# Performance work log

Hardware: AMD Instinct MI355X
Metric: run time of the kernel (lower is better)

The kernel has to match this reference:

```python
import jax, jax.numpy as jnp
import numpy as np

T, D = 256, 256
N, F, DM, H1, H2 = T + D, 2048, 512, 128, 64
E_HALF = T * D            # edges with src < dst (track -> detection)
LAM, SLACK = 5.0, -0.2    # hardcoded in original forward
SINK_ITERS = 8


def setup_inputs() -> dict:
    key = jax.random.key(0)
    ks = jax.random.split(key, 16)
    x = jax.random.normal(ks[0], (N, F), jnp.float32)
    coords = jax.random.normal(ks[1], (N, 4), jnp.float32)
    # boxes in xyxy with positive extent for IoU
    c = jax.random.uniform(ks[2], (N, 2), jnp.float32) * 0.8
    wh = jax.random.uniform(ks[3], (N, 2), jnp.float32) * 0.2 + 0.01
    coords_original = jnp.concatenate([c, c + wh], axis=1)
    ground_truth = (jax.random.uniform(ks[4], (E_HALF,)) < 0.1).astype(jnp.float32)
    # full bipartite directed edges: first half track->det (src<dst), second half reversed
    t = jnp.arange(T, dtype=jnp.int32)
    d = jnp.arange(D, dtype=jnp.int32) + T
    src_h = jnp.repeat(t, D)
    dst_h = jnp.tile(d, T)
    edge_index = jnp.stack([jnp.concatenate([src_h, dst_h]),
                            jnp.concatenate([dst_h, src_h])])

    def w(k, shape, fan_in):
        return jax.random.normal(k, shape, jnp.float32) / np.sqrt(fan_in).astype(np.float32)

    params = dict(
        W_enc=w(ks[5], (F, DM), F), b_enc=jnp.zeros((DM,), jnp.float32),
        app_W1=w(ks[6], (2 * DM, H1), 2 * DM), app_b1=jnp.zeros((H1,), jnp.float32),
        app_w2=w(ks[7], (H1,), H1), app_b2=jnp.zeros((), jnp.float32),
        geo_W1=w(ks[8], (8, H2), 8), geo_b1=jnp.zeros((H2,), jnp.float32),
        geo_w2=w(ks[9], (H2,), H2), geo_b2=jnp.zeros((), jnp.float32),
        aff_w=w(ks[10], (2,), 2), aff_b=jnp.zeros((), jnp.float32),
        W_self=w(ks[11], (DM, DM), DM), W_nbr=w(ks[12], (DM, DM), DM),
        b_mp=jnp.zeros((DM,), jnp.float32),
        fin_w=w(ks[13], (2,), 2), fin_b=jnp.zeros((), jnp.float32),
    )
    return dict(x=x, coords=coords, coords_original=coords_original,
                ground_truth=ground_truth, edge_index=edge_index, **params)


def _box_iou(a, b):
    # a, b: [E, 4] xyxy boxes
    lt = jnp.maximum(a[:, :2], b[:, :2])
    rb = jnp.minimum(a[:, 2:], b[:, 2:])
    wh = jnp.clip(rb - lt, 0.0)
    inter = wh[:, 0] * wh[:, 1]
    area_a = (a[:, 2] - a[:, 0]) * (a[:, 3] - a[:, 1])
    area_b = (b[:, 2] - b[:, 0]) * (b[:, 3] - b[:, 1])
    return inter / (area_a + area_b - inter + 1e-6)


def _forward(x, coords, coords_original, edge_index,
             W_enc, b_enc, app_W1, app_b1, app_w2, app_b2,
             geo_W1, geo_b1, geo_w2, geo_b2, aff_w, aff_b,
             W_self, W_nbr, b_mp, fin_w, fin_b):
    src, dst = edge_index[0], edge_index[1]
    # EncoderCNN -> node embeddings [N, DM]
    h = jax.nn.relu(x @ W_enc + b_enc)
    hs, hd = h[src], h[dst]                       # per-edge gathers [E, DM]
    # appearance affinity MLP on concat embeddings -> scalar per edge
    x1 = jax.nn.sigmoid(jax.nn.relu(jnp.concatenate([hs, hd], 1) @ app_W1 + app_b1) @ app_w2 + app_b2)
    # geometric affinity MLP on concat coords -> scalar per edge
    geo = jnp.concatenate([coords[src], coords[dst]], 1)   # [E, 8]
    x2 = jax.nn.sigmoid(jax.nn.relu(geo @ geo_W1 + geo_b1) @ geo_w2 + geo_b2)
    iou = _box_iou(coords_original[src], coords_original[dst])   # [E]
    # combine -> edge weight (affinityNet)
    ew = jax.nn.sigmoid(jnp.stack([x1, x2], axis=-1) @ aff_w + aff_b)  # [E]
    # optimNet: weighted message passing -> updated node embeddings
    agg = jax.ops.segment_sum(ew[:, None] * (hs @ W_nbr), dst, num_segments=N)
    out = jax.nn.relu(h @ W_self + agg + b_mp)    # [N, DM]
    # edges with src < dst are exactly the first E_HALF by construction
    a, b = out[src[:E_HALF]], out[dst[:E_HALF]]
    na = jnp.clip(jnp.linalg.norm(a, axis=1), 1e-6)
    nb = jnp.clip(jnp.linalg.norm(b, axis=1), 1e-6)
    cos = jnp.sum(a * b, axis=1) / (na * nb)
    fin = jax.nn.sigmoid(jnp.stack([cos, iou[:E_HALF]], axis=-1) @ fin_w + fin_b)  # [E_HALF]
    # scatter-built cost matrix with slack row/column, Sinkhorn normalization
    sv = jnp.exp(jnp.float32(SLACK * LAM))
    M = jnp.zeros((T + 1, D + 1), jnp.float32)
    M = M.at[src[:E_HALF], dst[:E_HALF] - T].set(jnp.exp(fin * LAM))
    M = M.at[:, D].set(sv)
    M = M.at[T, :].set(sv)
    for _ in range(SINK_ITERS):
        M = M / jnp.sum(M, axis=1, keepdims=True)
        M = M / jnp.sum(M, axis=0, keepdims=True)
    return M[:T, :D].reshape(-1)   # [T*D]


def reference(x, coords, coords_original, ground_truth, edge_index,
              W_enc, b_enc, app_W1, app_b1, app_w2, app_b2,
              geo_W1, geo_b1, geo_w2, geo_b2, aff_w, aff_b,
              W_self, W_nbr, b_mp, fin_w, fin_b):
    normalized = _forward(x, coords, coords_original, edge_index,
                          W_enc, b_enc, app_W1, app_b1, app_w2, app_b2,
                          geo_W1, geo_b1, geo_w2, geo_b2, aff_w, aff_b,
                          W_self, W_nbr, b_mp, fin_w, fin_b)
    # post-Sinkhorn entries are strictly positive, so the !=0 filter is identity
    det_num = jnp.full((1,), D, jnp.int32)
    tracklet_num = jnp.full((1,), T, jnp.int32)
    return normalized, ground_truth, det_num, tracklet_num
```

## Files before the change

kernel.cpp:

```cpp
#include <hip/hip_runtime.h>
#include <hip/hip_fp16.h>
#include <math.h>

#define EH   65536
#define LAMF 5.0f
#define SVF  0.36787944117144233f

typedef __bf16 bf16x8 __attribute__((ext_vector_type(8)));
typedef float  f32x4  __attribute__((ext_vector_type(4)));
typedef _Float16 f16x2 __attribute__((ext_vector_type(2)));

__device__ __forceinline__ float sigmoidf_(float x) { return 1.0f / (1.0f + expf(-x)); }

__device__ __forceinline__ void cvt1(float v, ushort& h, ushort& l) {
    __bf16 bh = (__bf16)v;
    h = __builtin_bit_cast(ushort, bh);
    __bf16 bl = (__bf16)(v - (float)bh);
    l = __builtin_bit_cast(ushort, bl);
}

__device__ __forceinline__ f16x2 u2h(uint u) { return __builtin_bit_cast(f16x2, u); }
__device__ __forceinline__ float2 h2f2u(uint u) {
    __half2 h = __builtin_bit_cast(__half2, u);
    return __half22float2(h);
}

#define LSTR 40
template<int MODE>
__global__ __launch_bounds__(256) void gemm64(
    const float* __restrict__ Aa, const float* __restrict__ Ab,
    const float* __restrict__ B0, const float* __restrict__ B1,
    const float* __restrict__ B2,
    const float* __restrict__ HsC45, const float* __restrict__ bmp,
    float* __restrict__ C0, float* __restrict__ C1)
{
    __shared__ ushort As_hi[64*LSTR], As_lo[64*LSTR], Bs_hi[64*LSTR], Bs_lo[64*LSTR];
    const int tid = threadIdx.x;
    const int row0 = blockIdx.y * 64;

    const float* Ap = Aa; int lda, arow0 = row0, ak = 0;
    const float* Bp; int ldb, kb = 0, bcol0;
    float* Cp; int ldc, ccol0;
    int KS;

    if (MODE == 0) {
        KS = 256; lda = 2048; ak = blockIdx.z * 256;
        Bp = B0; ldb = 512; kb = blockIdx.z * 256; bcol0 = blockIdx.x * 64;
        Cp = C0 + blockIdx.z * 262144; ldc = 512; ccol0 = bcol0;
    } else if (MODE == 1) {
        KS = 512; lda = 512;
        int cb = blockIdx.x;
        if (cb < 8)       { Bp=B0; ldb=512; kb=0;   bcol0=cb*64;        Cp=C0; ldc=1024; ccol0=cb*64; }
        else if (cb < 16) { Bp=B1; ldb=512; kb=0;   bcol0=(cb-8)*64;    Cp=C0; ldc=1024; ccol0=512+(cb-8)*64; }
        else if (cb < 18) { Bp=B2; ldb=128; kb=0;   bcol0=(cb-16)*64;   Cp=C1; ldc=256;  ccol0=(cb-16)*64; }
        else              { Bp=B2; ldb=128; kb=512; bcol0=(cb-18)*64;   Cp=C1; ldc=256;  ccol0=128+(cb-18)*64; }
    } else {
        KS = 256; lda = 256;
        if (row0 < 256) { Ap = Aa; arow0 = row0;       kb = 256; }
        else            { Ap = Ab; arow0 = row0 - 256; kb = 0; }
        Bp = B0; ldb = 1024; bcol0 = blockIdx.x * 64;
        Cp = C0; ldc = 512; ccol0 = bcol0;
    }

    const int arow = tid >> 2, kq = (tid & 3) * 8;
    const int kr = (tid & 15) * 2, nc0 = (tid >> 4) * 4;
    const float* aptr = Ap + (size_t)(arow0 + arow) * lda + ak + kq;
    const float* bptr = Bp + (size_t)(kb + kr) * ldb + bcol0 + nc0;

    f32x4 acc[2][2] = {};
    const int lane = tid & 63, w = tid >> 6;
    const int qr = (w >> 1) * 32, qc = (w & 1) * 32;
    const int fr = lane & 15, kg = (lane >> 4) * 8;

    float4 pa0, pa1, pb0, pb1;
    pa0 = *(const float4*)aptr; pa1 = *(const float4*)(aptr + 4);
    pb0 = *(const float4*)bptr; pb1 = *(const float4*)(bptr + ldb);

    for (int k0 = 0; k0 < KS; k0 += 32) {
        {
            ushort4 h0, l0, h1, l1;
            cvt1(pa0.x,h0.x,l0.x); cvt1(pa0.y,h0.y,l0.y); cvt1(pa0.z,h0.z,l0.z); cvt1(pa0.w,h0.w,l0.w);
            cvt1(pa1.x,h1.x,l1.x); cvt1(pa1.y,h1.y,l1.y); cvt1(pa1.z,h1.z,l1.z); cvt1(pa1.w,h1.w,l1.w);
            *(ushort4*)&As_hi[arow*LSTR + kq]     = h0;
            *(ushort4*)&As_hi[arow*LSTR + kq + 4] = h1;
            *(ushort4*)&As_lo[arow*LSTR + kq]     = l0;
            *(ushort4*)&As_lo[arow*LSTR + kq + 4] = l1;
            float b0a[4] = {pb0.x, pb0.y, pb0.z, pb0.w};
            float b1a[4] = {pb1.x, pb1.y, pb1.z, pb1.w};
            #pragma unroll
            for (int j = 0; j < 4; ++j) {
                ushort ha, la, hb, lb;
                cvt1(b0a[j], ha, la); cvt1(b1a[j], hb, lb);
                *(uint*)&Bs_hi[(nc0+j)*LSTR + kr] = (uint)ha | ((uint)hb << 16);
                *(uint*)&Bs_lo[(nc0+j)*LSTR + kr] = (uint)la | ((uint)lb << 16);
            }
        }
        __syncthreads();
        if (k0 + 32 < KS) {
            pa0 = *(const float4*)(aptr + k0 + 32);
            pa1 = *(const float4*)(aptr + k0 + 36);
            const float* bp2 = bptr + (size_t)(k0 + 32) * ldb;
            pb0 = *(const float4*)bp2; pb1 = *(const float4*)(bp2 + ldb);
        }
        bf16x8 ah[2], al[2], bh[2], bl[2];
        #pragma unroll
        for (int m = 0; m < 2; ++m) {
            int r = (qr + m*16 + fr) * LSTR + kg;
            ah[m] = *(const bf16x8*)&As_hi[r];
            al[m] = *(const bf16x8*)&As_lo[r];
        }
        #pragma unroll
        for (int n = 0; n < 2; ++n) {
            int r = (qc + n*16 + fr) * LSTR + kg;
            bh[n] = *(const bf16x8*)&Bs_hi[r];
            bl[n] = *(const bf16x8*)&Bs_lo[r];
        }
        #pragma unroll
        for (int m = 0; m < 2; ++m)
            #pragma unroll
            for (int n = 0; n < 2; ++n) {
                acc[m][n] = __builtin_amdgcn_mfma_f32_16x16x32_bf16(ah[m], bh[n], acc[m][n], 0, 0, 0);
                acc[m][n] = __builtin_amdgcn_mfma_f32_16x16x32_bf16(ah[m], bl[n], acc[m][n], 0, 0, 0);
                acc[m][n] = __builtin_amdgcn_mfma_f32_16x16x32_bf16(al[m], bh[n], acc[m][n], 0, 0, 0);
            }
        __syncthreads();
    }

    const int rbase = (lane >> 4) * 4;
    #pragma unroll
    for (int m = 0; m < 2; ++m)
        #pragma unroll
        for (int n = 0; n < 2; ++n)
            #pragma unroll
            for (int r = 0; r < 4; ++r) {
                int gr = row0 + qr + m*16 + rbase + r;
                int gc = ccol0 + qc + n*16 + (lane & 15);
                float v = acc[m][n][r];
                if (MODE == 2) {
                    v += HsC45[(size_t)gr * 1024 + 512 + gc] + bmp[gc];
                    v = fmaxf(v, 0.f);
                }
                Cp[(size_t)gr * ldc + gc] = v;
            }
}

__global__ __launch_bounds__(256) void enc_reduce(const float* __restrict__ P,
    const float* __restrict__ bias, float* __restrict__ h)
{
    int e = (blockIdx.x * 256 + threadIdx.x) * 4;
    int col = e & 511;
    float4 s = *(const float4*)&P[e];
    #pragma unroll
    for (int z = 1; z < 8; ++z) {
        float4 v = *(const float4*)&P[e + z * 262144];
        s.x += v.x; s.y += v.y; s.z += v.z; s.w += v.w;
    }
    float4 b = *(const float4*)&bias[col];
    float4 o;
    o.x = fmaxf(s.x + b.x, 0.f);
    o.y = fmaxf(s.y + b.y, 0.f);
    o.z = fmaxf(s.z + b.z, 0.f);
    o.w = fmaxf(s.w + b.w, 0.f);
    *(float4*)&h[e] = o;
}

__global__ __launch_bounds__(256) void edge_geo_kernel(
    const float* __restrict__ C23, const float* __restrict__ coords,
    const float* __restrict__ geo_W1, const float* __restrict__ geo_b1,
    const float* __restrict__ app_b1, const float* __restrict__ app_w2,
    const float* __restrict__ app_b2, const float* __restrict__ geo_w2,
    const float* __restrict__ geo_b2, const float* __restrict__ aff_w,
    const float* __restrict__ aff_b, const float* __restrict__ co,
    const float* __restrict__ gt, float* __restrict__ outp,
    float* __restrict__ ewT0, float* __restrict__ ew2, float* __restrict__ iou1)
{
    __shared__ __align__(16) float sA[16][132], sB[16][132];
    __shared__ __align__(16) float sGA[16][68], sGB[16][68];
    __shared__ __align__(16) float sw2[128], sgw2[64];
    __shared__ float sgw[8][64], sgb[64], scs[16][4], scd[16][4];
    const int tid = threadIdx.x;
    const int half = blockIdx.z;
    const int t0 = blockIdx.y * 16, d0 = blockIdx.x * 16;
    const int sbase = half ? (256 + d0) : t0;
    const int dbase = half ? t0 : (256 + d0);

    if (half == 1) {
        int bid = blockIdx.y * 16 + blockIdx.x;
        if (tid < 64) {
            int o = bid * 256 + tid * 4;
            *(float4*)&outp[EH + o] = *(const float4*)&gt[o];
        }
        if (bid == 0 && tid == 64) {
            outp[2 * EH]     = 256.0f;
            outp[2 * EH + 1] = 256.0f;
        }
    }

    for (int i = tid; i < 16 * 32; i += 256) {
        int rr = i >> 5, c4 = (i & 31) << 2;
        float4 va = *(const float4*)&C23[(sbase + rr) * 256 + c4];
        sA[rr][c4] = va.x; sA[rr][c4+1] = va.y; sA[rr][c4+2] = va.z; sA[rr][c4+3] = va.w;
        float4 vb = *(const float4*)&C23[(dbase + rr) * 256 + 128 + c4];
        float4 b1 = *(const float4*)&app_b1[c4];
        sB[rr][c4] = vb.x + b1.x; sB[rr][c4+1] = vb.y + b1.y;
        sB[rr][c4+2] = vb.z + b1.z; sB[rr][c4+3] = vb.w + b1.w;
    }
    for (int i = tid; i < 512; i += 256) sgw[i >> 6][i & 63] = geo_W1[i];
    if (tid < 64) sgb[tid] = geo_b1[tid];
    else if (tid < 192) sw2[tid - 64] = app_w2[tid - 64];
    else sgw2[tid - 192] = geo_w2[tid - 192];
    if (tid < 64) scs[tid >> 2][tid & 3] = coords[(sbase + (tid >> 2)) * 4 + (tid & 3)];
    else if (tid < 128) { int i = tid - 64; scd[i >> 2][i & 3] = coords[(dbase + (i >> 2)) * 4 + (i & 3)]; }
    __syncthreads();
    for (int v = tid; v < 2048; v += 256) {
        int hh = v >> 10, rr = (v >> 6) & 15, j = v & 63;
        if (hh == 0) {
            sGA[rr][j] = scs[rr][0]*sgw[0][j] + scs[rr][1]*sgw[1][j]
                       + scs[rr][2]*sgw[2][j] + scs[rr][3]*sgw[3][j] + sgb[j];
        } else {
            sGB[rr][j] = scd[rr][0]*sgw[4][j] + scd[rr][1]*sgw[5][j]
                       + scd[rr][2]*sgw[6][j] + scd[rr][3]*sgw[7][j];
        }
    }
    __syncthreads();
    const int tx = tid & 15, ty = tid >> 4;
    const int si = half ? tx : ty;
    const int di = half ? ty : tx;
    float acc1 = 0.f;
    #pragma unroll
    for (int j4 = 0; j4 < 128; j4 += 4) {
        float4 a = *(const float4*)&sA[si][j4];
        float4 b = *(const float4*)&sB[di][j4];
        float4 wv = *(const float4*)&sw2[j4];
        acc1 += fmaxf(a.x + b.x, 0.f) * wv.x + fmaxf(a.y + b.y, 0.f) * wv.y
              + fmaxf(a.z + b.z, 0.f) * wv.z + fmaxf(a.w + b.w, 0.f) * wv.w;
    }
    float x1 = sigmoidf_(acc1 + app_b2[0]);
    float acc2 = 0.f;
    #pragma unroll
    for (int j4 = 0; j4 < 64; j4 += 4) {
        float4 a = *(const float4*)&sGA[si][j4];
        float4 b = *(const float4*)&sGB[di][j4];
        float4 wv = *(const float4*)&sgw2[j4];
        acc2 += fmaxf(a.x + b.x, 0.f) * wv.x + fmaxf(a.y + b.y, 0.f) * wv.y
              + fmaxf(a.z + b.z, 0.f) * wv.z + fmaxf(a.w + b.w, 0.f) * wv.w;
    }
    float x2 = sigmoidf_(acc2 + geo_b2[0]);
    float e = sigmoidf_(x1 * aff_w[0] + x2 * aff_w[1] + aff_b[0]);
    const int t = t0 + ty, d = d0 + tx;
    if (half) ew2[t * 256 + d] = e;
    else      ewT0[d * 256 + t] = e;
    if (half == 0) {
        float4 a = *(const float4*)&co[t * 4];
        float4 b = *(const float4*)&co[(256 + d) * 4];
        float ltx = fmaxf(a.x, b.x), lty = fmaxf(a.y, b.y);
        float rbx = fminf(a.z, b.z), rby = fminf(a.w, b.w);
        float w  = fmaxf(rbx - ltx, 0.f), hh = fmaxf(rby - lty, 0.f);
        float inter = w * hh;
        float areaA = (a.z - a.x) * (a.w - a.y);
        float areaB = (b.z - b.x) * (b.w - b.y);
        iou1[t * 256 + d] = inter / (areaA + areaB - inter + 1e-6f);
    }
}

__global__ __launch_bounds__(256) void gram32(const float* __restrict__ outm,
    const float* __restrict__ iou, const float* __restrict__ finw,
    const float* __restrict__ finb, __half* __restrict__ Mh)
{
    __shared__ ushort As_hi[32*LSTR], As_lo[32*LSTR], Bs_hi[32*LSTR], Bs_lo[32*LSTR];
    __shared__ float snA[32], snB[32];
    const int tid = threadIdx.x;
    const int t0 = blockIdx.y * 32, d0 = blockIdx.x * 32;
    const float* Asrc = outm;
    const float* Bsrc = outm + (size_t)256 * 512;

    const int arow = tid >> 3, kq = (tid & 7) * 4;
    const float* aptr = Asrc + (size_t)(t0 + arow) * 512 + kq;
    const float* bptr = Bsrc + (size_t)(d0 + arow) * 512 + kq;

    f32x4 acc = {};
    float ssA = 0.f, ssB = 0.f;
    const int lane = tid & 63, w = tid >> 6;
    const int qr = (w >> 1) * 16, qc = (w & 1) * 16;
    const int fr = lane & 15, kg = (lane >> 4) * 8;

    float4 pa = *(const float4*)aptr;
    float4 pb = *(const float4*)bptr;

    for (int k0 = 0; k0 < 512; k0 += 32) {
        ssA += pa.x*pa.x + pa.y*pa.y + pa.z*pa.z + pa.w*pa.w;
        ssB += pb.x*pb.x + pb.y*pb.y + pb.z*pb.z + pb.w*pb.w;
        {
            ushort4 h4, l4;
            cvt1(pa.x,h4.x,l4.x); cvt1(pa.y,h4.y,l4.y); cvt1(pa.z,h4.z,l4.z); cvt1(pa.w,h4.w,l4.w);
            *(ushort4*)&As_hi[arow*LSTR + kq] = h4;
            *(ushort4*)&As_lo[arow*LSTR + kq] = l4;
            cvt1(pb.x,h4.x,l4.x); cvt1(pb.y,h4.y,l4.y); cvt1(pb.z,h4.z,l4.z); cvt1(pb.w,h4.w,l4.w);
            *(ushort4*)&Bs_hi[arow*LSTR + kq] = h4;
            *(ushort4*)&Bs_lo[arow*LSTR + kq] = l4;
        }
        __syncthreads();
        if (k0 + 32 < 512) {
            pa = *(const float4*)(aptr + k0 + 32);
            pb = *(const float4*)(bptr + k0 + 32);
        }
        bf16x8 ah, al, bh, bl;
        {
            int r = (qr + fr) * LSTR + kg;
            ah = *(const bf16x8*)&As_hi[r]; al = *(const bf16x8*)&As_lo[r];
        }
        {
            int r = (qc + fr) * LSTR + kg;
            bh = *(const bf16x8*)&Bs_hi[r]; bl = *(const bf16x8*)&Bs_lo[r];
        }
        acc = __builtin_amdgcn_mfma_f32_16x16x32_bf16(ah, bh, acc, 0, 0, 0);
        acc = __builtin_amdgcn_mfma_f32_16x16x32_bf16(ah, bl, acc, 0, 0, 0);
        acc = __builtin_amdgcn_mfma_f32_16x16x32_bf16(al, bh, acc, 0, 0, 0);
        __syncthreads();
    }
    ssA += __shfl_xor(ssA, 1); ssA += __shfl_xor(ssA, 2); ssA += __shfl_xor(ssA, 4);
    ssB += __shfl_xor(ssB, 1); ssB += __shfl_xor(ssB, 2); ssB += __shfl_xor(ssB, 4);
    if ((tid & 7) == 0) { snA[arow] = ssA; snB[arow] = ssB; }
    __syncthreads();
    const float fw0 = finw[0], fw1 = finw[1], fb = finb[0];
    const int rbase = (lane >> 4) * 4, lc = qc + (lane & 15);
    #pragma unroll
    for (int r = 0; r < 4; ++r) {
        int lr = qr + rbase + r;
        float na = fmaxf(sqrtf(snA[lr]), 1e-6f);
        float nb = fmaxf(sqrtf(snB[lc]), 1e-6f);
        int t = t0 + lr, d = d0 + lc;
        float cosv = acc[r] / (na * nb);
        float fin = sigmoidf_(cosv * fw0 + iou[t * 256 + d] * fw1 + fb);
        Mh[t * 256 + d] = __float2half(expf(fin * LAMF));
    }
}

__global__ __launch_bounds__(1024, 4) void sinkhorn4f(const __half* __restrict__ Mh,
    float* __restrict__ out)
{
    __shared__ __align__(16) float r_f[256], c_f[256];
    __shared__ float red[16];
    __shared__ __half r_h[256], c_h[256];
    const int tid = threadIdx.x;
    const int row = tid >> 2, sub4 = tid & 3;
    const int cg = tid >> 5, sub32 = tid & 31;

    const uint4* gm = (const uint4*)Mh;
    uint4 mr[8];
    #pragma unroll
    for (int j = 0; j < 8; ++j) mr[j] = gm[row * 32 + sub4 * 8 + j];
    uint4 mca[4], mcb[4];
    #pragma unroll
    for (int p = 0; p < 4; ++p) {
        int rp = 2 * sub32 + 64 * p;
        mca[p] = gm[rp * 32 + cg];
        mcb[p] = gm[(rp + 1) * 32 + cg];
    }
    if (tid < 256) { c_f[tid] = 1.0f; c_h[tid] = __float2half(1.0f); }
    if (tid == 0) red[1] = 1.0f / SVF;
    __syncthreads();

    const int b4 = (sub32 >> 4) & 1, b3 = (sub32 >> 3) & 1, b2 = (sub32 >> 2) & 1;

    for (int it = 0; it < 8; ++it) {
        float c256 = 1.0f / (SVF * red[1]);
        float a0 = 0.f, a1 = 0.f, a2 = 0.f, a3 = 0.f;
        {
            uint4 cu[4];
            #pragma unroll
            for (int j = 0; j < 4; ++j) cu[j] = *(const uint4*)&c_h[sub4 * 64 + j * 8];
            #pragma unroll
// ... 18 lines not shown
        if (tid < 64) {
            float s = c_f[tid] + c_f[tid + 64] + c_f[tid + 128] + c_f[tid + 192];
            #pragma unroll
            for (int o = 32; o; o >>= 1) s += __shfl_down(s, o);
            if (tid == 0) red[0] = s + c256;
        }
        if (sub4 == 0) {
            float v = 1.0f / (acc + SVF * c256);
            r_f[row] = v; r_h[row] = __float2half(v);
        }
        __syncthreads();

        float r256 = 1.0f / (SVF * red[0]);
        float b[8] = {0.f,0.f,0.f,0.f,0.f,0.f,0.f,0.f};
        #pragma unroll
        for (int p = 0; p < 4; ++p) {
            f16x2 rp = u2h(*(const uint*)&r_h[2 * sub32 + 64 * p]);
            uint lo, hi;
            lo = __builtin_amdgcn_perm(mcb[p].x, mca[p].x, 0x05040100);
            hi = __builtin_amdgcn_perm(mcb[p].x, mca[p].x, 0x07060302);
            b[0] = __builtin_amdgcn_fdot2(u2h(lo), rp, b[0], false);
            b[1] = __builtin_amdgcn_fdot2(u2h(hi), rp, b[1], false);
            lo = __builtin_amdgcn_perm(mcb[p].y, mca[p].y, 0x05040100);
            hi = __builtin_amdgcn_perm(mcb[p].y, mca[p].y, 0x07060302);
            b[2] = __builtin_amdgcn_fdot2(u2h(lo), rp, b[2], false);
            b[3] = __builtin_amdgcn_fdot2(u2h(hi), rp, b[3], false);
            lo = __builtin_amdgcn_perm(mcb[p].z, mca[p].z, 0x05040100);
            hi = __builtin_amdgcn_perm(mcb[p].z, mca[p].z, 0x07060302);
            b[4] = __builtin_amdgcn_fdot2(u2h(lo), rp, b[4], false);
            b[5] = __builtin_amdgcn_fdot2(u2h(hi), rp, b[5], false);
            lo = __builtin_amdgcn_perm(mcb[p].w, mca[p].w, 0x05040100);
            hi = __builtin_amdgcn_perm(mcb[p].w, mca[p].w, 0x07060302);
            b[6] = __builtin_amdgcn_fdot2(u2h(lo), rp, b[6], false);
            b[7] = __builtin_amdgcn_fdot2(u2h(hi), rp, b[7], false);
        }
        float t0v, t1v, t2v, t3v;
        t0v = b4 ? b[0] : b[4]; t1v = b4 ? b[1] : b[5];
        t2v = b4 ? b[2] : b[6]; t3v = b4 ? b[3] : b[7];
        t0v = __shfl_xor(t0v, 16); t1v = __shfl_xor(t1v, 16);
        t2v = __shfl_xor(t2v, 16); t3v = __shfl_xor(t3v, 16);
        float k0 = (b4 ? b[4] : b[0]) + t0v;
        float k1 = (b4 ? b[5] : b[1]) + t1v;
        float k2 = (b4 ? b[6] : b[2]) + t2v;
        float k3 = (b4 ? b[7] : b[3]) + t3v;
        float u0 = b3 ? k0 : k2, u1 = b3 ? k1 : k3;
        u0 = __shfl_xor(u0, 8); u1 = __shfl_xor(u1, 8);
        float m0 = (b3 ? k2 : k0) + u0;
        float m1 = (b3 ? k3 : k1) + u1;
        float w0 = b2 ? m0 : m1;
        w0 = __shfl_xor(w0, 4);
        float s = (b2 ? m1 : m0) + w0;
        s += __shfl_xor(s, 1); s += __shfl_xor(s, 2);
        if (tid < 64) {
            float s2 = r_f[tid] + r_f[tid + 64] + r_f[tid + 128] + r_f[tid + 192];
            #pragma unroll
            for (int o = 32; o; o >>= 1) s2 += __shfl_down(s2, o);
            if (tid == 0) red[1] = s2 + r256;
        }
        if ((sub32 & 3) == 0) {
            int col = cg * 8 + b4 * 4 + b3 * 2 + b2;
            float v = 1.0f / (s + SVF * r256);
            c_f[col] = v; c_h[col] = __float2half(v);
        }
        __syncthreads();
    }

    float rv = r_f[row];
    #pragma unroll
    for (int j = 0; j < 8; ++j) {
        int cb = sub4 * 64 + j * 8;
        float4 ca  = *(const float4*)&c_f[cb];
        float4 cb4 = *(const float4*)&c_f[cb + 4];
        float2 f0 = h2f2u(mr[j].x), f1 = h2f2u(mr[j].y);
        float2 f2 = h2f2u(mr[j].z), f3 = h2f2u(mr[j].w);
        float4 o0, o1;
        o0.x = f0.x * rv * ca.x;  o0.y = f0.y * rv * ca.y;
        o0.z = f1.x * rv * ca.z;  o0.w = f1.y * rv * ca.w;
        o1.x = f2.x * rv * cb4.x; o1.y = f2.y * rv * cb4.y;
        o1.z = f3.x * rv * cb4.z; o1.w = f3.y * rv * cb4.w;
        *(float4*)&out[row * 256 + cb]     = o0;
        *(float4*)&out[row * 256 + cb + 4] = o1;
    }
}

extern "C" void kernel_launch(void* const* d_in, const int* in_sizes, int n_in,
                              void* d_out, int out_size, void* d_ws, size_t ws_size,
                              hipStream_t stream)
{
    const float* x       = (const float*)d_in[0];
    const float* coords  = (const float*)d_in[1];
    const float* co      = (const float*)d_in[2];
    const float* gt      = (const float*)d_in[3];
    const float* W_enc   = (const float*)d_in[5];
    const float* b_enc   = (const float*)d_in[6];
    const float* app_W1  = (const float*)d_in[7];
    const float* app_b1  = (const float*)d_in[8];
    const float* app_w2  = (const float*)d_in[9];
    const float* app_b2  = (const float*)d_in[10];
    const float* geo_W1  = (const float*)d_in[11];
    const float* geo_b1  = (const float*)d_in[12];
    const float* geo_w2  = (const float*)d_in[13];
    const float* geo_b2  = (const float*)d_in[14];
    const float* aff_w   = (const float*)d_in[15];
    const float* aff_b   = (const float*)d_in[16];
    const float* W_self  = (const float*)d_in[17];
    const float* W_nbr   = (const float*)d_in[18];
    const float* b_mp    = (const float*)d_in[19];
    const float* fin_w   = (const float*)d_in[20];
    const float* fin_b   = (const float*)d_in[21];
    float* out = (float*)d_out;

    char* W = (char*)d_ws;
    float*  P     = (float*)(W + 0);
    float*  h     = (float*)(W + 8388608);
    float*  C45   = (float*)(W + 0);
    float*  C23   = (float*)(W + 2097152);
    float*  ewT0  = (float*)(W + 2621440);
    float*  ew2   = (float*)(W + 2883584);
    float*  iou1  = (float*)(W + 3145728);
    __half* Mh    = (__half*)(W + 3407872);
    float*  outm  = (float*)(W + 3670016);

    gemm64<0><<<dim3(8, 8, 8), 256, 0, stream>>>(x, nullptr, W_enc, nullptr, nullptr,
        nullptr, nullptr, P, nullptr);
    enc_reduce<<<256, 256, 0, stream>>>(P, b_enc, h);
    gemm64<1><<<dim3(20, 8), 256, 0, stream>>>(h, nullptr, W_nbr, W_self, app_W1,
        nullptr, nullptr, C45, C23);
    edge_geo_kernel<<<dim3(16, 16, 2), 256, 0, stream>>>(C23, coords, geo_W1, geo_b1,
        app_b1, app_w2, app_b2, geo_w2, geo_b2, aff_w, aff_b, co, gt, out,
        ewT0, ew2, iou1);
    gemm64<2><<<dim3(8, 8), 256, 0, stream>>>(ew2, ewT0, C45, nullptr, nullptr,
        C45, b_mp, outm, nullptr);
    gram32<<<dim3(8, 8), 256, 0, stream>>>(outm, iou1, fin_w, fin_b, Mh);
    sinkhorn4f<<<1, 1024, 0, stream>>>(Mh, out);
}
```

Before: 90.96 us.

## Fuse pipeline stages into one cooperative persistent kernel with grid syncs

```diff
diff --git a/kernel.cpp b/kernel.cpp
--- a/kernel.cpp
+++ b/kernel.cpp
@@ -1,6 +1,9 @@
 #include <hip/hip_runtime.h>
+#include <hip/hip_cooperative_groups.h>
 #include <hip/hip_fp16.h>
 #include <math.h>
+
+namespace cg = cooperative_groups;
 
 #define EH   65536
 #define LAMF 5.0f
@@ -26,46 +29,62 @@
 }
 
 #define LSTR 40
+
+struct GemmS {
+    ushort As_hi[64*LSTR], As_lo[64*LSTR], Bs_hi[64*LSTR], Bs_lo[64*LSTR];
+};
+struct EdgeS {
+    float sA[16][132], sB[16][132];
+    float sGA[16][68], sGB[16][68];
+    float sw2[128], sgw2[64];
+    float sgw[8][64], sgb[64];
+    float scs[16][4], scd[16][4];
+};
+struct GramS {
+    ushort As_hi[32*LSTR], As_lo[32*LSTR], Bs_hi[32*LSTR], Bs_lo[32*LSTR];
+    float snA[32], snB[32];
+};
+#define SMEM_BYTES 29184
+
 template<int MODE>
-__global__ __launch_bounds__(256) void gemm64(
+__device__ void gemm_phase(char* smem_, int bid,
     const float* __restrict__ Aa, const float* __restrict__ Ab,
     const float* __restrict__ B0, const float* __restrict__ B1,
-    const float* __restrict__ B2,
+    const float* __restrict__ B2, const float* __restrict__ bias,
     const float* __restrict__ HsC45, const float* __restrict__ bmp,
     float* __restrict__ C0, float* __restrict__ C1)
 {
-    __shared__ ushort As_hi[64*LSTR], As_lo[64*LSTR], Bs_hi[64*LSTR], Bs_lo[64*LSTR];
+    GemmS* S = (GemmS*)smem_;
     const int tid = threadIdx.x;
-    const int row0 = blockIdx.y * 64;
-
-    const float* Ap = Aa; int lda, arow0 = row0, ak = 0;
-    const float* Bp; int ldb, kb = 0, bcol0;
-    float* Cp; int ldc, ccol0;
-    int KS;
+
+    int row0, arow0, ak = 0, kb = 0, bcol0, ldb, ldc, ccol0, KS, lda;
+    const float* Ap = Aa; const float* Bp; float* Cp;
 
     if (MODE == 0) {
-        KS = 256; lda = 2048; ak = blockIdx.z * 256;
-        Bp = B0; ldb = 512; kb = blockIdx.z * 256; bcol0 = blockIdx.x * 64;
-        Cp = C0 + blockIdx.z * 262144; ldc = 512; ccol0 = bcol0;
+        int z = bid >> 6, by = (bid >> 3) & 7, bx = bid & 7;
+        row0 = by * 64; arow0 = row0; KS = 512; lda = 2048; ak = z * 512;
+        Bp = B0; ldb = 512; kb = z * 512; bcol0 = bx * 64;
+        Cp = C0 + z * 262144; ldc = 512; ccol0 = bcol0;
     } else if (MODE == 1) {
-        KS = 512; lda = 512;
-        int cb = blockIdx.x;
-        if (cb < 8)       { Bp=B0; ldb=512; kb=0;   bcol0=cb*64;        Cp=C0; ldc=1024; ccol0=cb*64; }
-        else if (cb < 16) { Bp=B1; ldb=512; kb=0;   bcol0=(cb-8)*64;    Cp=C0; ldc=1024; ccol0=512+(cb-8)*64; }
-        else if (cb < 18) { Bp=B2; ldb=128; kb=0;   bcol0=(cb-16)*64;   Cp=C1; ldc=256;  ccol0=(cb-16)*64; }
-        else              { Bp=B2; ldb=128; kb=512; bcol0=(cb-18)*64;   Cp=C1; ldc=256;  ccol0=128+(cb-18)*64; }
+        int by = bid / 20, cb = bid % 20;
+        row0 = by * 64; arow0 = row0; KS = 512; lda = 512;
+        if (cb < 8)       { Bp=B0; ldb=512; kb=0;   bcol0=cb*64;      Cp=C0; ldc=1024; ccol0=cb*64; }
+        else if (cb < 16) { Bp=B1; ldb=512; kb=0;   bcol0=(cb-8)*64;  Cp=C0; ldc=1024; ccol0=512+(cb-8)*64; }
+        else if (cb < 18) { Bp=B2; ldb=128; kb=0;   bcol0=(cb-16)*64; Cp=C1; ldc=256;  ccol0=(cb-16)*64; }
+        else              { Bp=B2; ldb=128; kb=512; bcol0=(cb-18)*64; Cp=C1; ldc=256;  ccol0=128+(cb-18)*64; }
     } else {
-        KS = 256; lda = 256;
+        int by = bid >> 3, bx = bid & 7;
+        row0 = by * 64; KS = 256; lda = 256;
         if (row0 < 256) { Ap = Aa; arow0 = row0;       kb = 256; }
         else            { Ap = Ab; arow0 = row0 - 256; kb = 0; }
-        Bp = B0; ldb = 1024; bcol0 = blockIdx.x * 64;
-        Cp = C0; ldc = 512; ccol0 = bcol0;
+        Bp = B0; ldb = 1024; bcol0 = bx * 64; Cp = C0; ldc = 512; ccol0 = bcol0;
     }
 
     const int arow = tid >> 2, kq = (tid & 3) * 8;
     const int kr = (tid & 15) * 2, nc0 = (tid >> 4) * 4;
-    const float* aptr = Ap + (size_t)(arow0 + arow) * lda + ak + kq;
-    const float* bptr = Bp + (size_t)(kb + kr) * ldb + bcol0 + nc0;
+    const float* aptr  = Ap + (size_t)(arow0 + arow) * lda + ak + kq;
+    const float* aptrP = Aa + (size_t)(arow0 + arow) * 512 + kq;
+    const float* bptr  = Bp + (size_t)(kb + kr) * ldb + bcol0 + nc0;
 
     f32x4 acc[2][2] = {};
     const int lane = tid & 63, w = tid >> 6;
@@ -73,32 +92,62 @@
     const int fr = lane & 15, kg = (lane >> 4) * 8;
 
     float4 pa0, pa1, pb0, pb1;
-    pa0 = *(const float4*)aptr; pa1 = *(const float4*)(aptr + 4);
+    float4 pz0[4], pz1[4];
+    if constexpr (MODE == 1) {
+        #pragma unroll
+        for (int z = 0; z < 4; ++z) {
+            pz0[z] = *(const float4*)(aptrP + z * 262144);
+            pz1[z] = *(const float4*)(aptrP + z * 262144 + 4);
+        }
+    } else {
+        pa0 = *(const float4*)aptr; pa1 = *(const float4*)(aptr + 4);
+    }
     pb0 = *(const float4*)bptr; pb1 = *(const float4*)(bptr + ldb);
 
     for (int k0 = 0; k0 < KS; k0 += 32) {
+        float4 sa0, sa1;
+        if constexpr (MODE == 1) {
+            float4 b0v = *(const float4*)&bias[k0 + kq];
+            float4 b1v = *(const float4*)&bias[k0 + kq + 4];
+            sa0.x = fmaxf(pz0[0].x + pz0[1].x + pz0[2].x + pz0[3].x + b0v.x, 0.f);
+            sa0.y = fmaxf(pz0[0].y + pz0[1].y + pz0[2].y + pz0[3].y + b0v.y, 0.f);
+            sa0.z = fmaxf(pz0[0].z + pz0[1].z + pz0[2].z + pz0[3].z + b0v.z, 0.f);
+            sa0.w = fmaxf(pz0[0].w + pz0[1].w + pz0[2].w + pz0[3].w + b0v.w, 0.f);
+            sa1.x = fmaxf(pz1[0].x + pz1[1].x + pz1[2].x + pz1[3].x + b1v.x, 0.f);
+            sa1.y = fmaxf(pz1[0].y + pz1[1].y + pz1[2].y + pz1[3].y + b1v.y, 0.f);
+            sa1.z = fmaxf(pz1[0].z + pz1[1].z + pz1[2].z + pz1[3].z + b1v.z, 0.f);
+            sa1.w = fmaxf(pz1[0].w + pz1[1].w + pz1[2].w + pz1[3].w + b1v.w, 0.f);
+        } else { sa0 = pa0; sa1 = pa1; }
         {
             ushort4 h0, l0, h1, l1;
-            cvt1(pa0.x,h0.x,l0.x); cvt1(pa0.y,h0.y,l0.y); cvt1(pa0.z,h0.z,l0.z); cvt1(pa0.w,h0.w,l0.w);
-            cvt1(pa1.x,h1.x,l1.x); cvt1(pa1.y,h1.y,l1.y); cvt1(pa1.z,h1.z,l1.z); cvt1(pa1.w,h1.w,l1.w);
-            *(ushort4*)&As_hi[arow*LSTR + kq]     = h0;
-            *(ushort4*)&As_hi[arow*LSTR + kq + 4] = h1;
-            *(ushort4*)&As_lo[arow*LSTR + kq]     = l0;
-            *(ushort4*)&As_lo[arow*LSTR + kq + 4] = l1;
+            cvt1(sa0.x,h0.x,l0.x); cvt1(sa0.y,h0.y,l0.y); cvt1(sa0.z,h0.z,l0.z); cvt1(sa0.w,h0.w,l0.w);
+            cvt1(sa1.x,h1.x,l1.x); cvt1(sa1.y,h1.y,l1.y); cvt1(sa1.z,h1.z,l1.z); cvt1(sa1.w,h1.w,l1.w);
+            *(ushort4*)&S->As_hi[arow*LSTR + kq]     = h0;
+            *(ushort4*)&S->As_hi[arow*LSTR + kq + 4] = h1;
+            *(ushort4*)&S->As_lo[arow*LSTR + kq]     = l0;
+            *(ushort4*)&S->As_lo[arow*LSTR + kq + 4] = l1;
             float b0a[4] = {pb0.x, pb0.y, pb0.z, pb0.w};
             float b1a[4] = {pb1.x, pb1.y, pb1.z, pb1.w};
             #pragma unroll
             for (int j = 0; j < 4; ++j) {
                 ushort ha, la, hb, lb;
                 cvt1(b0a[j], ha, la); cvt1(b1a[j], hb, lb);
-                *(uint*)&Bs_hi[(nc0+j)*LSTR + kr] = (uint)ha | ((uint)hb << 16);
-                *(uint*)&Bs_lo[(nc0+j)*LSTR + kr] = (uint)la | ((uint)lb << 16);
+                *(uint*)&S->Bs_hi[(nc0+j)*LSTR + kr] = (uint)ha | ((uint)hb << 16);
+                *(uint*)&S->Bs_lo[(nc0+j)*LSTR + kr] = (uint)la | ((uint)lb << 16);
             }
         }
         __syncthreads();
         if (k0 + 32 < KS) {
-            pa0 = *(const float4*)(aptr + k0 + 32);
-            pa1 = *(const float4*)(aptr + k0 + 36);
+            if constexpr (MODE == 1) {
+                #pragma unroll
+                for (int z = 0; z < 4; ++z) {
+                    pz0[z] = *(const float4*)(aptrP + z * 262144 + k0 + 32);
+                    pz1[z] = *(const float4*)(aptrP + z * 262144 + k0 + 36);
+                }
+            } else {
+                pa0 = *(const float4*)(aptr + k0 + 32);
+                pa1 = *(const float4*)(aptr + k0 + 36);
+            }
             const float* bp2 = bptr + (size_t)(k0 + 32) * ldb;
             pb0 = *(const float4*)bp2; pb1 = *(const float4*)(bp2 + ldb);
         }
@@ -106,14 +155,14 @@
         #pragma unroll
         for (int m = 0; m < 2; ++m) {
             int r = (qr + m*16 + fr) * LSTR + kg;
-            ah[m] = *(const bf16x8*)&As_hi[r];
-            al[m] = *(const bf16x8*)&As_lo[r];
+            ah[m] = *(const bf16x8*)&S->As_hi[r];
+            al[m] = *(const bf16x8*)&S->As_lo[r];
         }
         #pragma unroll
         for (int n = 0; n < 2; ++n) {
             int r = (qc + n*16 + fr) * LSTR + kg;
-            bh[n] = *(const bf16x8*)&Bs_hi[r];
-            bl[n] = *(const bf16x8*)&Bs_lo[r];
+            bh[n] = *(const bf16x8*)&S->Bs_hi[r];
+            bl[n] = *(const bf16x8*)&S->Bs_lo[r];
         }
         #pragma unroll
         for (int m = 0; m < 2; ++m)
@@ -144,27 +193,7 @@
             }
 }
 
-__global__ __launch_bounds__(256) void enc_reduce(const float* __restrict__ P,
-    const float* __restrict__ bias, float* __restrict__ h)
-{
-    int e = (blockIdx.x * 256 + threadIdx.x) * 4;
-    int col = e & 511;
-    float4 s = *(const float4*)&P[e];
-    #pragma unroll
-    for (int z = 1; z < 8; ++z) {
-        float4 v = *(const float4*)&P[e + z * 262144];
-        s.x += v.x; s.y += v.y; s.z += v.z; s.w += v.w;
-    }
-    float4 b = *(const float4*)&bias[col];
-    float4 o;
-    o.x = fmaxf(s.x + b.x, 0.f);
-    o.y = fmaxf(s.y + b.y, 0.f);
-    o.z = fmaxf(s.z + b.z, 0.f);
-    o.w = fmaxf(s.w + b.w, 0.f);
-    *(float4*)&h[e] = o;
-}
-
-__global__ __launch_bounds__(256) void edge_geo_kernel(
+__device__ void edge_phase(char* smem_, int bid,
     const float* __restrict__ C23, const float* __restrict__ coords,
     const float* __restrict__ geo_W1, const float* __restrict__ geo_b1,
     const float* __restrict__ app_b1, const float* __restrict__ app_w2,
@@ -174,103 +203,100 @@
     const float* __restrict__ gt, float* __restrict__ outp,
     float* __restrict__ ewT0, float* __restrict__ ew2, float* __restrict__ iou1)
 {
-    __shared__ __align__(16) float sA[16][132], sB[16][132];
-    __shared__ __align__(16) float sGA[16][68], sGB[16][68];
-    __shared__ __align__(16) float sw2[128], sgw2[64];
-    __shared__ float sgw[8][64], sgb[64], scs[16][4], scd[16][4];
+    EdgeS* S = (EdgeS*)smem_;
     const int tid = threadIdx.x;
-    const int half = blockIdx.z;
-    const int t0 = blockIdx.y * 16, d0 = blockIdx.x * 16;
-    const int sbase = half ? (256 + d0) : t0;
-    const int dbase = half ? t0 : (256 + d0);
-
-    if (half == 1) {
-        int bid = blockIdx.y * 16 + blockIdx.x;
-        if (tid < 64) {
-            int o = bid * 256 + tid * 4;
-            *(float4*)&outp[EH + o] = *(const float4*)&gt[o];
-        }
-        if (bid == 0 && tid == 64) {
-            outp[2 * EH]     = 256.0f;
-            outp[2 * EH + 1] = 256.0f;
-        }
-    }
-
-    for (int i = tid; i < 16 * 32; i += 256) {
-        int rr = i >> 5, c4 = (i & 31) << 2;
-        float4 va = *(const float4*)&C23[(sbase + rr) * 256 + c4];
-        sA[rr][c4] = va.x; sA[rr][c4+1] = va.y; sA[rr][c4+2] = va.z; sA[rr][c4+3] = va.w;
-        float4 vb = *(const float4*)&C23[(dbase + rr) * 256 + 128 + c4];
-        float4 b1 = *(const float4*)&app_b1[c4];
-        sB[rr][c4] = vb.x + b1.x; sB[rr][c4+1] = vb.y + b1.y;
-        sB[rr][c4+2] = vb.z + b1.z; sB[rr][c4+3] = vb.w + b1.w;
-    }
-    for (int i = tid; i < 512; i += 256) sgw[i >> 6][i & 63] = geo_W1[i];
-    if (tid < 64) sgb[tid] = geo_b1[tid];
-    else if (tid < 192) sw2[tid - 64] = app_w2[tid - 64];
-    else sgw2[tid - 192] = geo_w2[tid - 192];
-    if (tid < 64) scs[tid >> 2][tid & 3] = coords[(sbase + (tid >> 2)) * 4 + (tid & 3)];
-    else if (tid < 128) { int i = tid - 64; scd[i >> 2][i & 3] = coords[(dbase + (i >> 2)) * 4 + (i & 3)]; }
-    __syncthreads();
-    for (int v = tid; v < 2048; v += 256) {
-        int hh = v >> 10, rr = (v >> 6) & 15, j = v & 63;
-        if (hh == 0) {
-            sGA[rr][j] = scs[rr][0]*sgw[0][j] + scs[rr][1]*sgw[1][j]
-                       + scs[rr][2]*sgw[2][j] + scs[rr][3]*sgw[3][j] + sgb[j];
-        } else {
-            sGB[rr][j] = scd[rr][0]*sgw[4][j] + scd[rr][1]*sgw[5][j]
-                       + scd[rr][2]*sgw[6][j] + scd[rr][3]*sgw[7][j];
-        }
-    }
-    __syncthreads();
+    const int t0 = (bid >> 4) * 16, d0 = (bid & 15) * 16;
+
+    if (tid < 64) {
+        int o = bid * 256 + tid * 4;
+        *(float4*)&outp[EH + o] = *(const float4*)&gt[o];
+    }
+    if (bid == 0 && tid == 64) {
+        outp[2 * EH]     = 256.0f;
+        outp[2 * EH + 1] = 256.0f;
+    }
+
+    for (int i = tid; i < 512; i += 256) S->sgw[i >> 6][i & 63] = geo_W1[i];
+    if (tid < 64) S->sgb[tid] = geo_b1[tid];
+    else if (tid < 192) S->sw2[tid - 64] = app_w2[tid - 64];
+    else S->sgw2[tid - 192] = geo_w2[tid - 192];
+
     const int tx = tid & 15, ty = tid >> 4;
-    const int si = half ? tx : ty;
-    const int di = half ? ty : tx;
-    float acc1 = 0.f;
-    #pragma unroll
-    for (int j4 = 0; j4 < 128; j4 += 4) {
-        float4 a = *(const float4*)&sA[si][j4];
-        float4 b = *(const float4*)&sB[di][j4];
-        float4 wv = *(const float4*)&sw2[j4];
-        acc1 += fmaxf(a.x + b.x, 0.f) * wv.x + fmaxf(a.y + b.y, 0.f) * wv.y
-              + fmaxf(a.z + b.z, 0.f) * wv.z + fmaxf(a.w + b.w, 0.f) * wv.w;
-    }
-    float x1 = sigmoidf_(acc1 + app_b2[0]);
-    float acc2 = 0.f;
-    #pragma unroll
-    for (int j4 = 0; j4 < 64; j4 += 4) {
-        float4 a = *(const float4*)&sGA[si][j4];
-        float4 b = *(const float4*)&sGB[di][j4];
-        float4 wv = *(const float4*)&sgw2[j4];
-        acc2 += fmaxf(a.x + b.x, 0.f) * wv.x + fmaxf(a.y + b.y, 0.f) * wv.y
-              + fmaxf(a.z + b.z, 0.f) * wv.z + fmaxf(a.w + b.w, 0.f) * wv.w;
-    }
-    float x2 = sigmoidf_(acc2 + geo_b2[0]);
-    float e = sigmoidf_(x1 * aff_w[0] + x2 * aff_w[1] + aff_b[0]);
-    const int t = t0 + ty, d = d0 + tx;
-    if (half) ew2[t * 256 + d] = e;
-    else      ewT0[d * 256 + t] = e;
-    if (half == 0) {
-        float4 a = *(const float4*)&co[t * 4];
-        float4 b = *(const float4*)&co[(256 + d) * 4];
-        float ltx = fmaxf(a.x, b.x), lty = fmaxf(a.y, b.y);
-        float rbx = fminf(a.z, b.z), rby = fminf(a.w, b.w);
-        float w  = fmaxf(rbx - ltx, 0.f), hh = fmaxf(rby - lty, 0.f);
-        float inter = w * hh;
-        float areaA = (a.z - a.x) * (a.w - a.y);
-        float areaB = (b.z - b.x) * (b.w - b.y);
-        iou1[t * 256 + d] = inter / (areaA + areaB - inter + 1e-6f);
-    }
-}
-
-__global__ __launch_bounds__(256) void gram32(const float* __restrict__ outm,
+    for (int half = 0; half < 2; ++half) {
+        const int sbase = half ? (256 + d0) : t0;
+        const int dbase = half ? t0 : (256 + d0);
+        if (half) __syncthreads();
+        for (int i = tid; i < 16 * 32; i += 256) {
+            int rr = i >> 5, c4 = (i & 31) << 2;
+            float4 va = *(const float4*)&C23[(sbase + rr) * 256 + c4];
+            S->sA[rr][c4] = va.x; S->sA[rr][c4+1] = va.y;
+            S->sA[rr][c4+2] = va.z; S->sA[rr][c4+3] = va.w;
+            float4 vb = *(const float4*)&C23[(dbase + rr) * 256 + 128 + c4];
+            float4 b1 = *(const float4*)&app_b1[c4];
+            S->sB[rr][c4] = vb.x + b1.x; S->sB[rr][c4+1] = vb.y + b1.y;
+            S->sB[rr][c4+2] = vb.z + b1.z; S->sB[rr][c4+3] = vb.w + b1.w;
+        }
+        if (tid < 64) S->scs[tid >> 2][tid & 3] = coords[(sbase + (tid >> 2)) * 4 + (tid & 3)];
+        else if (tid < 128) { int i = tid - 64; S->scd[i >> 2][i & 3] = coords[(dbase + (i >> 2)) * 4 + (i & 3)]; }
+        __syncthreads();
+        for (int v = tid; v < 2048; v += 256) {
+            int hh = v >> 10, rr = (v >> 6) & 15, j = v & 63;
+            if (hh == 0) {
+                S->sGA[rr][j] = S->scs[rr][0]*S->sgw[0][j] + S->scs[rr][1]*S->sgw[1][j]
+                              + S->scs[rr][2]*S->sgw[2][j] + S->scs[rr][3]*S->sgw[3][j] + S->sgb[j];
+            } else {
+                S->sGB[rr][j] = S->scd[rr][0]*S->sgw[4][j] + S->scd[rr][1]*S->sgw[5][j]
+                              + S->scd[rr][2]*S->sgw[6][j] + S->scd[rr][3]*S->sgw[7][j];
+            }
+        }
+        __syncthreads();
+        const int si = half ? tx : ty;
+        const int di = half ? ty : tx;
+        float acc1 = 0.f;
+        #pragma unroll
+        for (int j4 = 0; j4 < 128; j4 += 4) {
+            float4 a = *(const float4*)&S->sA[si][j4];
+            float4 b = *(const float4*)&S->sB[di][j4];
+            float4 wv = *(const float4*)&S->sw2[j4];
+            acc1 += fmaxf(a.x + b.x, 0.f) * wv.x + fmaxf(a.y + b.y, 0.f) * wv.y
+                  + fmaxf(a.z + b.z, 0.f) * wv.z + fmaxf(a.w + b.w, 0.f) * wv.w;
+        }
+        float x1 = sigmoidf_(acc1 + app_b2[0]);
+        float acc2 = 0.f;
+        #pragma unroll
+        for (int j4 = 0; j4 < 64; j4 += 4) {
+            float4 a = *(const float4*)&S->sGA[si][j4];
+            float4 b = *(const float4*)&S->sGB[di][j4];
+            float4 wv = *(const float4*)&S->sgw2[j4];
+            acc2 += fmaxf(a.x + b.x, 0.f) * wv.x + fmaxf(a.y + b.y, 0.f) * wv.y
+                  + fmaxf(a.z + b.z, 0.f) * wv.z + fmaxf(a.w + b.w, 0.f) * wv.w;
+        }
+        float x2 = sigmoidf_(acc2 + geo_b2[0]);
+        float e = sigmoidf_(x1 * aff_w[0] + x2 * aff_w[1] + aff_b[0]);
+        const int t = t0 + ty, d = d0 + tx;
+        if (half) ew2[t * 256 + d] = e;
+        else      ewT0[d * 256 + t] = e;
+        if (half == 0) {
+            float4 a = *(const float4*)&co[t * 4];
+            float4 b = *(const float4*)&co[(256 + d) * 4];
+            float ltx = fmaxf(a.x, b.x), lty = fmaxf(a.y, b.y);
+            float rbx = fminf(a.z, b.z), rby = fminf(a.w, b.w);
+            float w  = fmaxf(rbx - ltx, 0.f), hh = fmaxf(rby - lty, 0.f);
+            float inter = w * hh;
+            float areaA = (a.z - a.x) * (a.w - a.y);
+            float areaB = (b.z - b.x) * (b.w - b.y);
+            iou1[t * 256 + d] = inter / (areaA + areaB - inter + 1e-6f);
+        }
+    }
+}
+
+__device__ void gram_phase(char* smem_, int bid, const float* __restrict__ outm,
     const float* __restrict__ iou, const float* __restrict__ finw,
     const float* __restrict__ finb, __half* __restrict__ Mh)
 {
-    __shared__ ushort As_hi[32*LSTR], As_lo[32*LSTR], Bs_hi[32*LSTR], Bs_lo[32*LSTR];
-    __shared__ float snA[32], snB[32];
+    GramS* S = (GramS*)smem_;
     const int tid = threadIdx.x;
-    const int t0 = blockIdx.y * 32, d0 = blockIdx.x * 32;
+    const int t0 = (bid >> 3) * 32, d0 = (bid & 7) * 32;
     const float* Asrc = outm;
     const float* Bsrc = outm + (size_t)256 * 512;
 
@@ -293,11 +319,11 @@
         {
             ushort4 h4, l4;
             cvt1(pa.x,h4.x,l4.x); cvt1(pa.y,h4.y,l4.y); cvt1(pa.z,h4.z,l4.z); cvt1(pa.w,h4.w,l4.w);
-            *(ushort4*)&As_hi[arow*LSTR + kq] = h4;
-            *(ushort4*)&As_lo[arow*LSTR + kq] = l4;
+            *(ushort4*)&S->As_hi[arow*LSTR + kq] = h4;
+            *(ushort4*)&S->As_lo[arow*LSTR + kq] = l4;
             cvt1(pb.x,h4.x,l4.x); cvt1(pb.y,h4.y,l4.y); cvt1(pb.z,h4.z,l4.z); cvt1(pb.w,h4.w,l4.w);
-            *(ushort4*)&Bs_hi[arow*LSTR + kq] = h4;
-            *(ushort4*)&Bs_lo[arow*LSTR + kq] = l4;
+            *(ushort4*)&S->Bs_hi[arow*LSTR + kq] = h4;
+            *(ushort4*)&S->Bs_lo[arow*LSTR + kq] = l4;
         }
         __syncthreads();
         if (k0 + 32 < 512) {
@@ -307,11 +333,11 @@
         bf16x8 ah, al, bh, bl;
         {
             int r = (qr + fr) * LSTR + kg;
-            ah = *(const bf16x8*)&As_hi[r]; al = *(const bf16x8*)&As_lo[r];
+            ah = *(const bf16x8*)&S->As_hi[r]; al = *(const bf16x8*)&S->As_lo[r];
         }
         {
             int r = (qc + fr) * LSTR + kg;
-            bh = *(const bf16x8*)&Bs_hi[r]; bl = *(const bf16x8*)&Bs_lo[r];
+            bh = *(const bf16x8*)&S->Bs_hi[r]; bl = *(const bf16x8*)&S->Bs_lo[r];
         }
         acc = __builtin_amdgcn_mfma_f32_16x16x32_bf16(ah, bh, acc, 0, 0, 0);
         acc = __builtin_amdgcn_mfma_f32_16x16x32_bf16(ah, bl, acc, 0, 0, 0);
@@ -320,20 +346,54 @@
     }
     ssA += __shfl_xor(ssA, 1); ssA += __shfl_xor(ssA, 2); ssA += __shfl_xor(ssA, 4);
     ssB += __shfl_xor(ssB, 1); ssB += __shfl_xor(ssB, 2); ssB += __shfl_xor(ssB, 4);
-    if ((tid & 7) == 0) { snA[arow] = ssA; snB[arow] = ssB; }
+    if ((tid & 7) == 0) { S->snA[arow] = ssA; S->snB[arow] = ssB; }
     __syncthreads();
     const float fw0 = finw[0], fw1 = finw[1], fb = finb[0];
     const int rbase = (lane >> 4) * 4, lc = qc + (lane & 15);
     #pragma unroll
     for (int r = 0; r < 4; ++r) {
         int lr = qr + rbase + r;
-        float na = fmaxf(sqrtf(snA[lr]), 1e-6f);
-        float nb = fmaxf(sqrtf(snB[lc]), 1e-6f);
+        float na = fmaxf(sqrtf(S->snA[lr]), 1e-6f);
+        float nb = fmaxf(sqrtf(S->snB[lc]), 1e-6f);
         int t = t0 + lr, d = d0 + lc;
         float cosv = acc[r] / (na * nb);
         float fin = sigmoidf_(cosv * fw0 + iou[t * 256 + d] * fw1 + fb);
         Mh[t * 256 + d] = __float2half(expf(fin * LAMF));
     }
+}
+
+struct MegaP {
+    const float *x, *coords, *co, *gt;
+    const float *W_enc, *b_enc, *app_W1, *app_b1, *app_w2, *app_b2;
+    const float *geo_W1, *geo_b1, *geo_w2, *geo_b2, *aff_w, *aff_b;
+    const float *W_self, *W_nbr, *b_mp, *fin_w, *fin_b;
+    float *P, *C45, *C23, *ewT0, *ew2, *iou1, *outm, *out;
+    __half *Mh;
+};
+
+__global__ __launch_bounds__(256) void mega_kernel(MegaP p)
+{
+    extern __shared__ char smem[];
+    cg::grid_group grid = cg::this_grid();
+    const int bid = blockIdx.x;
+
+    gemm_phase<0>(smem, bid, p.x, nullptr, p.W_enc, nullptr, nullptr,
+                  nullptr, nullptr, nullptr, p.P, nullptr);
+    grid.sync();
+    if (bid < 160)
+        gemm_phase<1>(smem, bid, p.P, nullptr, p.W_nbr, p.W_self, p.app_W1,
+                      p.b_enc, nullptr, nullptr, p.C45, p.C23);
+    grid.sync();
+    edge_phase(smem, bid, p.C23, p.coords, p.geo_W1, p.geo_b1, p.app_b1,
+               p.app_w2, p.app_b2, p.geo_w2, p.geo_b2, p.aff_w, p.aff_b,
+               p.co, p.gt, p.out, p.ewT0, p.ew2, p.iou1);
+    grid.sync();
+    if (bid < 64)
+        gemm_phase<2>(smem, bid, p.ew2, p.ewT0, p.C45, nullptr, nullptr,
+                      nullptr, p.C45, p.b_mp, p.outm, nullptr);
+    grid.sync();
+    if (bid < 64)
+        gram_phase(smem, bid, p.outm, p.iou1, p.fin_w, p.fin_b, p.Mh);
 }
 
 __global__ __launch_bounds__(1024, 4) void sinkhorn4f(const __half* __restrict__ Mh,
@@ -344,7 +404,7 @@
     __shared__ __half r_h[256], c_h[256];
     const int tid = threadIdx.x;
     const int row = tid >> 2, sub4 = tid & 3;
-    const int cg = tid >> 5, sub32 = tid & 31;
+    const int cg_ = tid >> 5, sub32 = tid & 31;
 
     const uint4* gm = (const uint4*)Mh;
     uint4 mr[8];
@@ -352,10 +412,10 @@
     for (int j = 0; j < 8; ++j) mr[j] = gm[row * 32 + sub4 * 8 + j];
     uint4 mca[4], mcb[4];
     #pragma unroll
-    for (int p = 0; p < 4; ++p) {
-        int rp = 2 * sub32 + 64 * p;
-        mca[p] = gm[rp * 32 + cg];
-        mcb[p] = gm[(rp + 1) * 32 + cg];
+    for (int pq = 0; pq < 4; ++pq) {
+        int rp = 2 * sub32 + 64 * pq;
+        mca[pq] = gm[rp * 32 + cg_];
+        mcb[pq] = gm[(rp + 1) * 32 + cg_];
     }
     if (tid < 256) { c_f[tid] = 1.0f; c_h[tid] = __float2half(1.0f); }
     if (tid == 0) red[1] = 1.0f / SVF;
@@ -404,23 +464,23 @@
         float r256 = 1.0f / (SVF * red[0]);
         float b[8] = {0.f,0.f,0.f,0.f,0.f,0.f,0.f,0.f};
         #pragma unroll
-        for (int p = 0; p < 4; ++p) {
-            f16x2 rp = u2h(*(const uint*)&r_h[2 * sub32 + 64 * p]);
+        for (int pq = 0; pq < 4; ++pq) {
+            f16x2 rp = u2h(*(const uint*)&r_h[2 * sub32 + 64 * pq]);
             uint lo, hi;
-            lo = __builtin_amdgcn_perm(mcb[p].x, mca[p].x, 0x05040100);
-            hi = __builtin_amdgcn_perm(mcb[p].x, mca[p].x, 0x07060302);
+            lo = __builtin_amdgcn_perm(mcb[pq].x, mca[pq].x, 0x05040100);
+            hi = __builtin_amdgcn_perm(mcb[pq].x, mca[pq].x, 0x07060302);
             b[0] = __builtin_amdgcn_fdot2(u2h(lo), rp, b[0], false);
             b[1] = __builtin_amdgcn_fdot2(u2h(hi), rp, b[1], false);
-            lo = __builtin_amdgcn_perm(mcb[p].y, mca[p].y, 0x05040100);
-            hi = __builtin_amdgcn_perm(mcb[p].y, mca[p].y, 0x07060302);
+            lo = __builtin_amdgcn_perm(mcb[pq].y, mca[pq].y, 0x05040100);
+            hi = __builtin_amdgcn_perm(mcb[pq].y, mca[pq].y, 0x07060302);
             b[2] = __builtin_amdgcn_fdot2(u2h(lo), rp, b[2], false);
             b[3] = __builtin_amdgcn_fdot2(u2h(hi), rp, b[3], false);
-            lo = __builtin_amdgcn_perm(mcb[p].z, mca[p].z, 0x05040100);
-            hi = __builtin_amdgcn_perm(mcb[p].z, mca[p].z, 0x07060302);
+            lo = __builtin_amdgcn_perm(mcb[pq].z, mca[pq].z, 0x05040100);
+            hi = __builtin_amdgcn_perm(mcb[pq].z, mca[pq].z, 0x07060302);
             b[4] = __builtin_amdgcn_fdot2(u2h(lo), rp, b[4], false);
             b[5] = __builtin_amdgcn_fdot2(u2h(hi), rp, b[5], false);
-            lo = __builtin_amdgcn_perm(mcb[p].w, mca[p].w, 0x05040100);
-            hi = __builtin_amdgcn_perm(mcb[p].w, mca[p].w, 0x07060302);
+            lo = __builtin_amdgcn_perm(mcb[pq].w, mca[pq].w, 0x05040100);
+            hi = __builtin_amdgcn_perm(mcb[pq].w, mca[pq].w, 0x07060302);
             b[6] = __builtin_amdgcn_fdot2(u2h(lo), rp, b[6], false);
             b[7] = __builtin_amdgcn_fdot2(u2h(hi), rp, b[7], false);
         }
@@ -448,7 +508,7 @@
             if (tid == 0) red[1] = s2 + r256;
         }
         if ((sub32 & 3) == 0) {
-            int col = cg * 8 + b4 * 4 + b3 * 2 + b2;
+            int col = cg_ * 8 + b4 * 4 + b3 * 2 + b2;
             float v = 1.0f / (s + SVF * r256);
             c_f[col] = v; c_h[col] = __float2half(v);
         }
@@ -477,50 +537,41 @@
                               void* d_out, int out_size, void* d_ws, size_t ws_size,
                               hipStream_t stream)
 {
-    const float* x       = (const float*)d_in[0];
-    const float* coords  = (const float*)d_in[1];
-    const float* co      = (const float*)d_in[2];
-    const float* gt      = (const float*)d_in[3];
-    const float* W_enc   = (const float*)d_in[5];
-    const float* b_enc   = (const float*)d_in[6];
-    const float* app_W1  = (const float*)d_in[7];
-    const float* app_b1  = (const float*)d_in[8];
-    const float* app_w2  = (const float*)d_in[9];
-    const float* app_b2  = (const float*)d_in[10];
-    const float* geo_W1  = (const float*)d_in[11];
-    const float* geo_b1  = (const float*)d_in[12];
-    const float* geo_w2  = (const float*)d_in[13];
-    const float* geo_b2  = (const float*)d_in[14];
-    const float* aff_w   = (const float*)d_in[15];
-    const float* aff_b   = (const float*)d_in[16];
-    const float* W_self  = (const float*)d_in[17];
-    const float* W_nbr   = (const float*)d_in[18];
-    const float* b_mp    = (const float*)d_in[19];
-    const float* fin_w   = (const float*)d_in[20];
-    const float* fin_b   = (const float*)d_in[21];
-    float* out = (float*)d_out;
-
     char* W = (char*)d_ws;
-    float*  P     = (float*)(W + 0);
-    float*  h     = (float*)(W + 8388608);
-    float*  C45   = (float*)(W + 0);
-    float*  C23   = (float*)(W + 2097152);
-    float*  ewT0  = (float*)(W + 2621440);
-    float*  ew2   = (float*)(W + 2883584);
-    float*  iou1  = (float*)(W + 3145728);
-    __half* Mh    = (__half*)(W + 3407872);
-    float*  outm  = (float*)(W + 3670016);
-
-    gemm64<0><<<dim3(8, 8, 8), 256, 0, stream>>>(x, nullptr, W_enc, nullptr, nullptr,
-        nullptr, nullptr, P, nullptr);
-    enc_reduce<<<256, 256, 0, stream>>>(P, b_enc, h);
-    gemm64<1><<<dim3(20, 8), 256, 0, stream>>>(h, nullptr, W_nbr, W_self, app_W1,
-        nullptr, nullptr, C45, C23);
-    edge_geo_kernel<<<dim3(16, 16, 2), 256, 0, stream>>>(C23, coords, geo_W1, geo_b1,
-        app_b1, app_w2, app_b2, geo_w2, geo_b2, aff_w, aff_b, co, gt, out,
-        ewT0, ew2, iou1);
-    gemm64<2><<<dim3(8, 8), 256, 0, stream>>>(ew2, ewT0, C45, nullptr, nullptr,
-        C45, b_mp, outm, nullptr);
-    gram32<<<dim3(8, 8), 256, 0, stream>>>(outm, iou1, fin_w, fin_b, Mh);
-    sinkhorn4f<<<1, 1024, 0, stream>>>(Mh, out);
-}
+    MegaP p;
+    p.x       = (const float*)d_in[0];
+    p.coords  = (const float*)d_in[1];
+    p.co      = (const float*)d_in[2];
+    p.gt      = (const float*)d_in[3];
+    p.W_enc   = (const float*)d_in[5];
+    p.b_enc   = (const float*)d_in[6];
+    p.app_W1  = (const float*)d_in[7];
+    p.app_b1  = (const float*)d_in[8];
+    p.app_w2  = (const float*)d_in[9];
+    p.app_b2  = (const float*)d_in[10];
+    p.geo_W1  = (const float*)d_in[11];
+    p.geo_b1  = (const float*)d_in[12];
+    p.geo_w2  = (const float*)d_in[13];
+    p.geo_b2  = (const float*)d_in[14];
+    p.aff_w   = (const float*)d_in[15];
+    p.aff_b   = (const float*)d_in[16];
+    p.W_self  = (const float*)d_in[17];
+    p.W_nbr   = (const float*)d_in[18];
+    p.b_mp    = (const float*)d_in[19];
+    p.fin_w   = (const float*)d_in[20];
+    p.fin_b   = (const float*)d_in[21];
+    p.out     = (float*)d_out;
+    p.P     = (float*)(W + 0);
+    p.C45   = (float*)(W + 4194304);
+    p.C23   = (float*)(W + 6291456);
+    p.ewT0  = (float*)(W + 6815744);
+    p.ew2   = (float*)(W + 7077888);
+    p.iou1  = (float*)(W + 7340032);
+    p.Mh    = (__half*)(W + 7596288);
+    p.outm  = (float*)(W + 7727104);
+
+    void* args[] = { &p };
+    hipLaunchCooperativeKernel((void*)mega_kernel, dim3(256), dim3(256),
+                               args, SMEM_BYTES, stream);
+    sinkhorn4f<<<1, 1024, 0, stream>>>(p.Mh, p.out);
+}
```

Result: slower. 233.2 us (+156.4%).
